# Optimization experiments

Measured on AMD Instinct MI355X. Metric: run time of the kernel, lower is better.

## Reference

```python
import jax, jax.numpy as jnp
import numpy as np

IN_DIM = 96
HIDDEN = 256
EPS = 1e-6
NEG = -1e10


def setup_inputs() -> dict:
    key = jax.random.key(0)
    ks = jax.random.split(key, 12)
    B, S = 8, 2048
    q = jax.random.normal(ks[0], (B, S, IN_DIM), dtype=jnp.float32)
    k = jax.random.normal(ks[1], (B, S, IN_DIM), dtype=jnp.float32)
    v = jax.random.normal(ks[2], (B, S, IN_DIM), dtype=jnp.float32)
    mask = jax.random.randint(ks[3], (B, S, S), 0, 2, dtype=jnp.int32)
    s = 1.0 / np.sqrt(IN_DIM)
    Wq = jax.random.normal(ks[4], (IN_DIM, HIDDEN), dtype=jnp.float32) * s
    bq = jax.random.normal(ks[5], (HIDDEN,), dtype=jnp.float32) * 0.01
    Wk = jax.random.normal(ks[6], (IN_DIM, HIDDEN), dtype=jnp.float32) * s
    bk = jax.random.normal(ks[7], (HIDDEN,), dtype=jnp.float32) * 0.01
    Wv = jax.random.normal(ks[8], (IN_DIM, HIDDEN), dtype=jnp.float32) * s
    bv = jax.random.normal(ks[9], (HIDDEN,), dtype=jnp.float32) * 0.01
    gamma = jnp.ones((HIDDEN,), dtype=jnp.float32)
    beta = jnp.zeros((HIDDEN,), dtype=jnp.float32)
    return {"query": q, "key": k, "value": v, "mask": mask,
            "Wq": Wq, "bq": bq, "Wk": Wk, "bk": bk, "Wv": Wv, "bv": bv,
            "gamma": gamma, "beta": beta}


def reference(query, key, value, mask, Wq, bq, Wk, bk, Wv, bv, gamma, beta):
    # Linear projections: [B,S,96] @ [96,H] -> [B,S,H]
    q = jnp.einsum('bsf,fh->bsh', query, Wq) + bq
    k = jnp.einsum('bsf,fh->bsh', key, Wk) + bk
    v = jnp.einsum('bsf,fh->bsh', value, Wv) + bv
    # Scaled dot-product scores: [B,S,S]
    score = jnp.einsum('bqh,bkh->bqk', q, k) / jnp.sqrt(jnp.float32(HIDDEN))
    score = jnp.where(mask == 0, jnp.float32(NEG), score)
    attn = jax.nn.softmax(score, axis=-1)
    out = jnp.einsum('bqk,bkh->bqh', attn, v)
    # LayerNorm over last dim, eps=1e-6
    mu = jnp.mean(out, axis=-1, keepdims=True)
    var = jnp.mean(jnp.square(out - mu), axis=-1, keepdims=True)
    normed = (out - mu) * jax.lax.rsqrt(var + EPS)
    return normed * gamma + beta
```

## Files before the change

### kernel.cpp

```cpp
#include <hip/hip_runtime.h>

#define B_   8
#define S_   2048
#define IN_  96
#define H_   256

typedef float    f32x4 __attribute__((ext_vector_type(4)));
typedef _Float16 f16x8 __attribute__((ext_vector_type(8)));

__device__ __forceinline__ unsigned short f2h(float x) {
    return __builtin_bit_cast(unsigned short, (_Float16)x);
}

__global__ __launch_bounds__(256) void wconv_kernel(
    const float* __restrict__ Wq, const float* __restrict__ Wk,
    const float* __restrict__ Wv, unsigned short* __restrict__ wt)
{
    const int p  = blockIdx.x >> 3;
    const int h0 = (blockIdx.x & 7) * 32;
    const float* W = (p == 0) ? Wq : (p == 1) ? Wk : Wv;
    unsigned short* dst = wt + (size_t)p * H_ * IN_ + (size_t)h0 * IN_;

    __shared__ unsigned short lds[32][100];
    const int t = threadIdx.x;
    #pragma unroll
    for (int i = 0; i < 12; ++i) {
        int idx = i * 256 + t;
        int f = idx >> 5;
        int hl = idx & 31;
        lds[hl][f] = f2h(W[f * H_ + h0 + hl]);
    }
    __syncthreads();
    #pragma unroll
    for (int j = 0; j < 6; ++j) {
        int e = (j * 256 + t) * 2;
        int hl = e / IN_, f = e % IN_;
        unsigned int pk = (unsigned int)lds[hl][f] |
                          ((unsigned int)lds[hl][f + 1] << 16);
        ((unsigned int*)dst)[j * 256 + t] = pk;
    }
}

__global__ __launch_bounds__(256) void proj_kernel3(
    const float* __restrict__ query, const float* __restrict__ key,
    const float* __restrict__ value, const unsigned short* __restrict__ wt,
    const float* __restrict__ bq, const float* __restrict__ bk,
    const float* __restrict__ bv,
    unsigned short* __restrict__ pq, unsigned short* __restrict__ pk,
    unsigned short* __restrict__ pv)
{
    __shared__ unsigned short Xs[3][16][104];

    const int t    = threadIdx.x;
    const int lane = t & 63;
    const int wave = t >> 6;
    const int col  = lane & 15;
    const int quad = lane >> 4;
    const int bi   = blockIdx.x;
    const int s0   = bi * 16;
    const int b    = s0 >> 11;
    const int sl   = s0 & (S_ - 1);

    const float* srcs[3] = { query + (size_t)s0 * IN_,
                             key   + (size_t)s0 * IN_,
                             value + (size_t)s0 * IN_ };
    #pragma unroll
    for (int p = 0; p < 3; ++p) {
        #pragma unroll
        for (int i = 0; i < 2; ++i) {
            int idx = i * 256 + t;
            if (idx < 384) {
                f32x4 x = *(const f32x4*)(srcs[p] + idx * 4);
                int r = idx / 24;
                int f = (idx - r * 24) * 4;
                unsigned long long pkk =
                    (unsigned long long)f2h(x[0])
                  | ((unsigned long long)f2h(x[1]) << 16)
                  | ((unsigned long long)f2h(x[2]) << 32)
                  | ((unsigned long long)f2h(x[3]) << 48);
                *(unsigned long long*)&Xs[p][r][f] = pkk;
            }
        }
    }
    __syncthreads();

    const int hc = wave;
    #pragma unroll
    for (int p = 0; p < 3; ++p) {
        const unsigned short* wbase = wt + (size_t)p * H_ * IN_;
        f16x8 wfr[4][3];
        #pragma unroll
        for (int ht = 0; ht < 4; ++ht)
            #pragma unroll
            for (int kc = 0; kc < 3; ++kc)
                wfr[ht][kc] = *(const f16x8*)(wbase
                    + (size_t)(hc * 64 + ht * 16 + col) * IN_ + kc * 32 + quad * 8);
        f16x8 xfr[3];
        #pragma unroll
        for (int kc = 0; kc < 3; ++kc)
            xfr[kc] = *(const f16x8*)&Xs[p][col][kc * 32 + quad * 8];

        f32x4 acc[4];
        #pragma unroll
        for (int ht = 0; ht < 4; ++ht) acc[ht] = (f32x4)(0.0f);
        #pragma unroll
        for (int kc = 0; kc < 3; ++kc)
            #pragma unroll
            for (int ht = 0; ht < 4; ++ht)
                acc[ht] = (p < 2)
                    ? __builtin_amdgcn_mfma_f32_16x16x32_f16(xfr[kc], wfr[ht][kc], acc[ht], 0, 0, 0)
                    : __builtin_amdgcn_mfma_f32_16x16x32_f16(wfr[ht][kc], xfr[kc], acc[ht], 0, 0, 0);

        if (p < 2) {
            unsigned short* dst  = (p == 0) ? pq : pk;
            const float*    bias = (p == 0) ? bq : bk;
            #pragma unroll
            for (int ht = 0; ht < 4; ++ht) {
                float bh = bias[hc * 64 + ht * 16 + col];
                const int s    = hc * 2 + (ht >> 1);
                const int lq   = ((ht & 1) * 2 + (col >> 3)) * 16;
                const int j    = col & 7;
                #pragma unroll
                for (int r = 0; r < 4; ++r)
                    dst[(size_t)(((bi * 8 + s) * 64 + lq + quad * 4 + r)) * 8 + j]
                        = f2h(acc[ht][r] + bh);
            }
        } else {
            const int kl  = (sl & 63) + col;
            const int c   = sl >> 6;
            const int s2  = kl >> 5;
            const int qv  = (kl >> 3) & 3;
            const int jj  = col & 7;
            #pragma unroll
            for (int ht = 0; ht < 4; ++ht) {
                f32x4 b4 = *(const f32x4*)(bv + hc * 64 + ht * 16 + quad * 4);
                #pragma unroll
                for (int r = 0; r < 4; ++r)
                    pv[(size_t)(((b * 32 + c) * 32 + hc * 8 + ht * 2 + s2) * 64
                                + qv * 16 + quad * 4 + r) * 8 + jj]
                        = f2h(acc[ht][r] + b4[r]);
            }
        }
    }
}

__global__ __launch_bounds__(256, 2) void attn_kernel(
    const unsigned short* __restrict__ pq, const unsigned short* __restrict__ pk,
    const unsigned short* __restrict__ pv, const int* __restrict__ mask,
    const float* __restrict__ gamma, const float* __restrict__ beta,
    float* __restrict__ out)
{
    __shared__ union {
        unsigned short P[2][32][68];
        float Obuf[32][260];
    } sm;
    __shared__ float lsum[4][32];

    const int tid  = threadIdx.x;
    const int wave = tid >> 6;
    const int lane = tid & 63;
    const int col  = lane & 15;
    const int quad = lane >> 4;

    const int b     = blockIdx.x & 7;
    const int strip = blockIdx.x >> 3;
    const int q0    = strip << 5;

    f16x8 qf[2][8];
    #pragma unroll
    for (int st = 0; st < 2; ++st) {
        const unsigned short* qb = pq + (size_t)(b * 128 + strip * 2 + st) * 4096
                                      + lane * 8;
        #pragma unroll
        for (int s = 0; s < 8; ++s) qf[st][s] = *(const f16x8*)(qb + s * 512);
    }

    f32x4 O[2][4];
    #pragma unroll
    for (int st = 0; st < 2; ++st)
        #pragma unroll
        for (int ht = 0; ht < 4; ++ht) O[st][ht] = (f32x4)(0.0f);
    float l0 = 0.0f, l1 = 0.0f;

    const unsigned short* pkb = pk + (size_t)(b * 128) * 4096 + lane * 8;
    const unsigned short* pvb = pv + (size_t)(b * 32) * 32 * 512
                                   + (size_t)wave * 8 * 512 + lane * 8;
    const int* mb0 = mask + (size_t)(b * S_ + q0 + col) * S_ + wave * 16 + quad * 4;
    const int* mb1 = mb0 + 16 * S_;

    f16x8 kf[2][8];
    #pragma unroll
    for (int s = 0; s < 8; ++s)
        kf[0][s] = *(const f16x8*)(pkb + (size_t)wave * 4096 + s * 512);

    int4 mc0 = *(const int4*)mb0;
    int4 mc1 = *(const int4*)mb1;

    #pragma unroll 2
    for (int c = 0; c < 32; ++c) {
        const int pb = c & 1;
        const int cn = (c < 31) ? c + 1 : c;

        const unsigned short* vb = pvb + (size_t)c * 32 * 512;
        f16x8 vf[4][2];
        #pragma unroll
        for (int ht = 0; ht < 4; ++ht)
            #pragma unroll
            for (int s2 = 0; s2 < 2; ++s2)
                vf[ht][s2] = *(const f16x8*)(vb + (size_t)(ht * 2 + s2) * 512);

        int4 mn0 = *(const int4*)(mb0 + cn * 64);
        int4 mn1 = *(const int4*)(mb1 + cn * 64);

        f32x4 St0 = (f32x4)(0.0f), St1 = (f32x4)(0.0f);
        #pragma unroll
        for (int s = 0; s < 8; ++s) {
            St0 = __builtin_amdgcn_mfma_f32_16x16x32_f16(kf[pb][s], qf[0][s], St0, 0, 0, 0);
            St1 = __builtin_amdgcn_mfma_f32_16x16x32_f16(kf[pb][s], qf[1][s], St1, 0, 0, 0);
        }

        {
            const unsigned short* kb = pkb + (size_t)(cn * 4 + wave) * 4096;
            #pragma unroll
            for (int s = 0; s < 8; ++s)
                kf[pb ^ 1][s] = *(const f16x8*)(kb + s * 512);
        }

        {
            int mi[4] = { mc0.x, mc0.y, mc0.z, mc0.w };
            unsigned long long pk64 = 0;
            #pragma unroll
            for (int r = 0; r < 4; ++r) {
                float p = (mi[r] == 0) ? 0.0f : __expf(St0[r] * 0.0625f - 6.0f);
                _Float16 ph = (_Float16)p;
                l0 += (float)ph;
                pk64 |= (unsigned long long)__builtin_bit_cast(unsigned short, ph)
                        << (16 * r);
            }
            *(unsigned long long*)&sm.P[pb][col][wave * 16 + quad * 4] = pk64;
        }
        {
            int mi[4] = { mc1.x, mc1.y, mc1.z, mc1.w };
            unsigned long long pk64 = 0;
            #pragma unroll
            for (int r = 0; r < 4; ++r) {
                float p = (mi[r] == 0) ? 0.0f : __expf(St1[r] * 0.0625f - 6.0f);
                _Float16 ph = (_Float16)p;
                l1 += (float)ph;
                pk64 |= (unsigned long long)__builtin_bit_cast(unsigned short, ph)
                        << (16 * r);
            }
            *(unsigned long long*)&sm.P[pb][16 + col][wave * 16 + quad * 4] = pk64;
        }
        mc0 = mn0; mc1 = mn1;

        __syncthreads();

        #pragma unroll
        for (int st = 0; st < 2; ++st) {
            #pragma unroll
            for (int s2 = 0; s2 < 2; ++s2) {
                union { unsigned long long u[2]; f16x8 v; } pu;
                const unsigned short* pr = &sm.P[pb][st * 16 + col][s2 * 32 + quad * 8];
                pu.u[0] = *(const unsigned long long*)pr;
                pu.u[1] = *(const unsigned long long*)(pr + 4);
                f16x8 pf = pu.v;
                #pragma unroll
                for (int ht = 0; ht < 4; ++ht)
                    O[st][ht] = __builtin_amdgcn_mfma_f32_16x16x32_f16(pf, vf[ht][s2], O[st][ht], 0, 0, 0);
            }
        }
    }

    l0 += __shfl_xor(l0, 16); l0 += __shfl_xor(l0, 32);
    l1 += __shfl_xor(l1, 16); l1 += __shfl_xor(l1, 32);
    if (lane < 16) { lsum[wave][lane] = l0; lsum[wave][16 + lane] = l1; }
    __syncthreads();

    #pragma unroll
    for (int st = 0; st < 2; ++st) {
        float ltot = lsum[0][st * 16 + col] + lsum[1][st * 16 + col]
                   + lsum[2][st * 16 + col] + lsum[3][st * 16 + col];
        float linv = 1.0f / ltot;
        float li4[4];
        #pragma unroll
        for (int r = 0; r < 4; ++r) li4[r] = __shfl(linv, quad * 4 + r);
        #pragma unroll
        for (int ht = 0; ht < 4; ++ht)
            #pragma unroll
            for (int r = 0; r < 4; ++r)
                sm.Obuf[st * 16 + quad * 4 + r][wave * 64 + ht * 16 + col]
                    = O[st][ht][r] * li4[r];
    }
    __syncthreads();

    #pragma unroll
    for (int st = 0; st < 2; ++st) {
        const int q = st * 16 + (tid >> 4);
        const int i = tid & 15;
        float vals[16];
        float sum = 0.0f;
        #pragma unroll
        for (int j = 0; j < 16; ++j) {
            vals[j] = sm.Obuf[q][j * 16 + i];
            sum += vals[j];
        }
        sum += __shfl_xor(sum, 1);
        sum += __shfl_xor(sum, 2);
        sum += __shfl_xor(sum, 4);
        sum += __shfl_xor(sum, 8);
        float mu = sum * (1.0f / H_);
        float sq = 0.0f;
        #pragma unroll
        for (int j = 0; j < 16; ++j) {
            float d = vals[j] - mu;
            sq += d * d;
        }
        sq += __shfl_xor(sq, 1);
        sq += __shfl_xor(sq, 2);
        sq += __shfl_xor(sq, 4);
        sq += __shfl_xor(sq, 8);
        float rstd = rsqrtf(sq * (1.0f / H_) + 1e-6f);

        float* orow = out + (size_t)(b * S_ + q0 + q) * H_;
        #pragma unroll
        for (int j = 0; j < 16; ++j) {
            int h = j * 16 + i;
            orow[h] = (vals[j] - mu) * rstd * gamma[h] + beta[h];
        }
    }
}

extern "C" void kernel_launch(void* const* d_in, const int* in_sizes, int n_in,
                              void* d_out, int out_size, void* d_ws, size_t ws_size,
                              hipStream_t stream)
{
    const float* query = (const float*)d_in[0];
    const float* key   = (const float*)d_in[1];
    const float* value = (const float*)d_in[2];
    const int*   mask  = (const int*)d_in[3];
    const float* Wq = (const float*)d_in[4];
    const float* bq = (const float*)d_in[5];
    const float* Wk = (const float*)d_in[6];
    const float* bk = (const float*)d_in[7];
    const float* Wv = (const float*)d_in[8];
    const float* bv = (const float*)d_in[9];
    const float* gamma = (const float*)d_in[10];
    const float* beta  = (const float*)d_in[11];
    float* out = (float*)d_out;

    const size_t NQK = (size_t)B_ * S_ * H_;
    unsigned short* pq = (unsigned short*)d_ws;
    unsigned short* pk = pq + NQK;
    unsigned short* pv = pk + NQK;
    unsigned short* wt = pv + NQK;

    wconv_kernel<<<24, 256, 0, stream>>>(Wq, Wk, Wv, wt);
    proj_kernel3<<<B_ * S_ / 16, 256, 0, stream>>>(query, key, value, wt,
                                                   bq, bk, bv, pq, pk, pv);
    attn_kernel<<<B_ * S_ / 32, 256, 0, stream>>>(pq, pk, pv, mask, gamma, beta, out);
}
```

Baseline: 304.4 us.

## Split attention over key halves and merge partials in a LayerNorm kernel

```diff
diff --git a/kernel.cpp b/kernel.cpp
--- a/kernel.cpp
+++ b/kernel.cpp
@@ -4,12 +4,24 @@
 #define S_   2048
 #define IN_  96
 #define H_   256
+#define NROW (B_ * S_)
 
 typedef float    f32x4 __attribute__((ext_vector_type(4)));
 typedef _Float16 f16x8 __attribute__((ext_vector_type(8)));
 
 __device__ __forceinline__ unsigned short f2h(float x) {
     return __builtin_bit_cast(unsigned short, (_Float16)x);
+}
+__device__ __forceinline__ float h2f(unsigned short x) {
+    return (float)__builtin_bit_cast(_Float16, x);
+}
+__device__ __forceinline__ int4 nt_load_int4(const int* p) {
+    long long v0 = __builtin_nontemporal_load((const long long*)p);
+    long long v1 = __builtin_nontemporal_load(((const long long*)p) + 1);
+    int4 r;
+    r.x = (int)(v0 & 0xffffffffLL); r.y = (int)(v0 >> 32);
+    r.z = (int)(v1 & 0xffffffffLL); r.w = (int)(v1 >> 32);
+    return r;
 }
 
 __global__ __launch_bounds__(256) void wconv_kernel(
@@ -147,13 +159,9 @@
 __global__ __launch_bounds__(256, 2) void attn_kernel(
     const unsigned short* __restrict__ pq, const unsigned short* __restrict__ pk,
     const unsigned short* __restrict__ pv, const int* __restrict__ mask,
-    const float* __restrict__ gamma, const float* __restrict__ beta,
-    float* __restrict__ out)
-{
-    __shared__ union {
-        unsigned short P[2][32][68];
-        float Obuf[32][260];
-    } sm;
+    unsigned short* __restrict__ Opart, float* __restrict__ lpart)
+{
+    __shared__ unsigned short P[2][32][68];
     __shared__ float lsum[4][32];
 
     const int tid  = threadIdx.x;
@@ -163,7 +171,8 @@
     const int quad = lane >> 4;
 
     const int b     = blockIdx.x & 7;
-    const int strip = blockIdx.x >> 3;
+    const int strip = (blockIdx.x >> 3) & 63;
+    const int kh    = blockIdx.x >> 9;
     const int q0    = strip << 5;
 
     f16x8 qf[2][8];
@@ -185,23 +194,25 @@
     const unsigned short* pkb = pk + (size_t)(b * 128) * 4096 + lane * 8;
     const unsigned short* pvb = pv + (size_t)(b * 32) * 32 * 512
                                    + (size_t)wave * 8 * 512 + lane * 8;
-    const int* mb0 = mask + (size_t)(b * S_ + q0 + col) * S_ + wave * 16 + quad * 4;
+    const int* mb0 = mask + (size_t)(b * S_ + q0 + col) * S_ + kh * 1024
+                   + wave * 16 + quad * 4;
     const int* mb1 = mb0 + 16 * S_;
 
     f16x8 kf[2][8];
     #pragma unroll
     for (int s = 0; s < 8; ++s)
-        kf[0][s] = *(const f16x8*)(pkb + (size_t)wave * 4096 + s * 512);
-
-    int4 mc0 = *(const int4*)mb0;
-    int4 mc1 = *(const int4*)mb1;
+        kf[0][s] = *(const f16x8*)(pkb + (size_t)(kh * 64 + wave) * 4096 + s * 512);
+
+    int4 mc0 = nt_load_int4(mb0);
+    int4 mc1 = nt_load_int4(mb1);
 
     #pragma unroll 2
-    for (int c = 0; c < 32; ++c) {
+    for (int c = 0; c < 16; ++c) {
         const int pb = c & 1;
-        const int cn = (c < 31) ? c + 1 : c;
-
-        const unsigned short* vb = pvb + (size_t)c * 32 * 512;
+        const int cn = (c < 15) ? c + 1 : c;
+        const int gc = kh * 16 + c;
+
+        const unsigned short* vb = pvb + (size_t)gc * 32 * 512;
         f16x8 vf[4][2];
         #pragma unroll
         for (int ht = 0; ht < 4; ++ht)
@@ -209,8 +220,8 @@
             for (int s2 = 0; s2 < 2; ++s2)
                 vf[ht][s2] = *(const f16x8*)(vb + (size_t)(ht * 2 + s2) * 512);
 
-        int4 mn0 = *(const int4*)(mb0 + cn * 64);
-        int4 mn1 = *(const int4*)(mb1 + cn * 64);
+        int4 mn0 = nt_load_int4(mb0 + cn * 64);
+        int4 mn1 = nt_load_int4(mb1 + cn * 64);
 
         f32x4 St0 = (f32x4)(0.0f), St1 = (f32x4)(0.0f);
         #pragma unroll
@@ -220,7 +231,7 @@
         }
 
         {
-            const unsigned short* kb = pkb + (size_t)(cn * 4 + wave) * 4096;
+            const unsigned short* kb = pkb + (size_t)(kh * 64 + cn * 4 + wave) * 4096;
             #pragma unroll
             for (int s = 0; s < 8; ++s)
                 kf[pb ^ 1][s] = *(const f16x8*)(kb + s * 512);
@@ -237,7 +248,7 @@
                 pk64 |= (unsigned long long)__builtin_bit_cast(unsigned short, ph)
                         << (16 * r);
             }
-            *(unsigned long long*)&sm.P[pb][col][wave * 16 + quad * 4] = pk64;
+            *(unsigned long long*)&P[pb][col][wave * 16 + quad * 4] = pk64;
         }
         {
             int mi[4] = { mc1.x, mc1.y, mc1.z, mc1.w };
@@ -250,7 +261,7 @@
                 pk64 |= (unsigned long long)__builtin_bit_cast(unsigned short, ph)
                         << (16 * r);
             }
-            *(unsigned long long*)&sm.P[pb][16 + col][wave * 16 + quad * 4] = pk64;
+            *(unsigned long long*)&P[pb][16 + col][wave * 16 + quad * 4] = pk64;
         }
         mc0 = mn0; mc1 = mn1;
 
@@ -261,7 +272,7 @@
             #pragma unroll
             for (int s2 = 0; s2 < 2; ++s2) {
                 union { unsigned long long u[2]; f16x8 v; } pu;
-                const unsigned short* pr = &sm.P[pb][st * 16 + col][s2 * 32 + quad * 8];
+                const unsigned short* pr = &P[pb][st * 16 + col][s2 * 32 + quad * 8];
                 pu.u[0] = *(const unsigned long long*)pr;
                 pu.u[1] = *(const unsigned long long*)(pr + 4);
                 f16x8 pf = pu.v;
@@ -277,57 +288,71 @@
     if (lane < 16) { lsum[wave][lane] = l0; lsum[wave][16 + lane] = l1; }
     __syncthreads();
 
-    #pragma unroll
-    for (int st = 0; st < 2; ++st) {
-        float ltot = lsum[0][st * 16 + col] + lsum[1][st * 16 + col]
-                   + lsum[2][st * 16 + col] + lsum[3][st * 16 + col];
-        float linv = 1.0f / ltot;
-        float li4[4];
-        #pragma unroll
-        for (int r = 0; r < 4; ++r) li4[r] = __shfl(linv, quad * 4 + r);
+    if (wave == 0 && lane < 16) {
+        #pragma unroll
+        for (int st = 0; st < 2; ++st) {
+            float lt = lsum[0][st * 16 + lane] + lsum[1][st * 16 + lane]
+                     + lsum[2][st * 16 + lane] + lsum[3][st * 16 + lane];
+            lpart[(size_t)kh * NROW + b * S_ + q0 + st * 16 + lane] = lt;
+        }
+    }
+
+    unsigned short* ob = Opart + (size_t)kh * NROW * H_ + (size_t)(b * S_) * H_;
+    #pragma unroll
+    for (int st = 0; st < 2; ++st)
         #pragma unroll
         for (int ht = 0; ht < 4; ++ht)
             #pragma unroll
             for (int r = 0; r < 4; ++r)
-                sm.Obuf[st * 16 + quad * 4 + r][wave * 64 + ht * 16 + col]
-                    = O[st][ht][r] * li4[r];
-    }
-    __syncthreads();
-
-    #pragma unroll
-    for (int st = 0; st < 2; ++st) {
-        const int q = st * 16 + (tid >> 4);
-        const int i = tid & 15;
-        float vals[16];
-        float sum = 0.0f;
-        #pragma unroll
-        for (int j = 0; j < 16; ++j) {
-            vals[j] = sm.Obuf[q][j * 16 + i];
-            sum += vals[j];
-        }
-        sum += __shfl_xor(sum, 1);
-        sum += __shfl_xor(sum, 2);
-        sum += __shfl_xor(sum, 4);
-        sum += __shfl_xor(sum, 8);
-        float mu = sum * (1.0f / H_);
-        float sq = 0.0f;
-        #pragma unroll
-        for (int j = 0; j < 16; ++j) {
-            float d = vals[j] - mu;
-            sq += d * d;
-        }
-        sq += __shfl_xor(sq, 1);
-        sq += __shfl_xor(sq, 2);
-        sq += __shfl_xor(sq, 4);
-        sq += __shfl_xor(sq, 8);
-        float rstd = rsqrtf(sq * (1.0f / H_) + 1e-6f);
-
-        float* orow = out + (size_t)(b * S_ + q0 + q) * H_;
-        #pragma unroll
-        for (int j = 0; j < 16; ++j) {
-            int h = j * 16 + i;
-            orow[h] = (vals[j] - mu) * rstd * gamma[h] + beta[h];
-        }
+                ob[(size_t)(q0 + st * 16 + quad * 4 + r) * H_
+                   + wave * 64 + ht * 16 + col] = f2h(O[st][ht][r]);
+}
+
+__global__ __launch_bounds__(256) void merge_ln_kernel(
+    const unsigned short* __restrict__ Opart, const float* __restrict__ lpart,
+    const float* __restrict__ gamma, const float* __restrict__ beta,
+    float* __restrict__ out)
+{
+    const int R0 = blockIdx.x * 16;
+    const int q  = threadIdx.x >> 4;
+    const int i  = threadIdx.x & 15;
+
+    const size_t row = (size_t)(R0 + q);
+    float linv = 1.0f / (lpart[row] + lpart[NROW + row]);
+
+    const unsigned short* o0 = Opart + row * H_;
+    const unsigned short* o1 = o0 + (size_t)NROW * H_;
+
+    float vals[16];
+    float sum = 0.0f;
+    #pragma unroll
+    for (int j = 0; j < 16; ++j) {
+        int h = j * 16 + i;
+        vals[j] = (h2f(o0[h]) + h2f(o1[h])) * linv;
+        sum += vals[j];
+    }
+    sum += __shfl_xor(sum, 1);
+    sum += __shfl_xor(sum, 2);
+    sum += __shfl_xor(sum, 4);
+    sum += __shfl_xor(sum, 8);
+    float mu = sum * (1.0f / H_);
+    float sq = 0.0f;
+    #pragma unroll
+    for (int j = 0; j < 16; ++j) {
+        float d = vals[j] - mu;
+        sq += d * d;
+    }
+    sq += __shfl_xor(sq, 1);
+    sq += __shfl_xor(sq, 2);
+    sq += __shfl_xor(sq, 4);
+    sq += __shfl_xor(sq, 8);
+    float rstd = rsqrtf(sq * (1.0f / H_) + 1e-6f);
+
+    float* orow = out + row * H_;
+    #pragma unroll
+    for (int j = 0; j < 16; ++j) {
+        int h = j * 16 + i;
+        orow[h] = (vals[j] - mu) * rstd * gamma[h] + beta[h];
     }
 }
 
@@ -354,9 +379,12 @@
     unsigned short* pk = pq + NQK;
     unsigned short* pv = pk + NQK;
     unsigned short* wt = pv + NQK;
+    unsigned short* Op = wt + (size_t)3 * H_ * IN_;
+    float*          lp = (float*)(Op + (size_t)2 * NROW * H_);
 
     wconv_kernel<<<24, 256, 0, stream>>>(Wq, Wk, Wv, wt);
     proj_kernel3<<<B_ * S_ / 16, 256, 0, stream>>>(query, key, value, wt,
                                                    bq, bk, bv, pq, pk, pv);
-    attn_kernel<<<B_ * S_ / 32, 256, 0, stream>>>(pq, pk, pv, mask, gamma, beta, out);
-}
+    attn_kernel<<<B_ * S_ / 32 * 2, 256, 0, stream>>>(pq, pk, pv, mask, Op, lp);
+    merge_ln_kernel<<<NROW / 16, 256, 0, stream>>>(Op, lp, gamma, beta, out);
+}
```

New measurement: 307.7 us. Within noise of the previous version (+1.1%).
